# Performance work log

Measured on AMD Instinct MI355X. Metric: run time of the kernel, lower is better.

The kernel has to match this reference:

```python
import jax, jax.numpy as jnp
import numpy as np

HEAD_SIZE = 64


def setup_inputs() -> dict:
    key = jax.random.key(0)
    ks = jax.random.split(key, 10)
    B, S, D, H, hs = 4, 2048, 768, 12, HEAD_SIZE
    F = 4 * D
    sd = lambda n: 1.0 / np.sqrt(n)
    return {
        "x": jax.random.normal(ks[0], (B, S, D), jnp.float32),
        "Wq": jax.random.normal(ks[1], (H, D, hs), jnp.float32) * sd(D),
        "Wk": jax.random.normal(ks[2], (H, D, hs), jnp.float32) * sd(D),
        "Wv": jax.random.normal(ks[3], (H, D, hs), jnp.float32) * sd(D),
        "Wo": jax.random.normal(ks[4], (D, D), jnp.float32) * sd(D),
        "bo": jnp.zeros((D,), jnp.float32),
        "W1": jax.random.normal(ks[5], (D, F), jnp.float32) * sd(D),
        "b1": jnp.zeros((F,), jnp.float32),
        "W2": jax.random.normal(ks[6], (F, D), jnp.float32) * sd(F),
        "b2": jnp.zeros((D,), jnp.float32),
    }


def reference(x, Wq, Wk, Wv, Wo, bo, W1, b1, W2, b2):
    B, S, D = x.shape
    hs = Wq.shape[-1]
    # per-head projections (no bias), vectorized over heads: [B,H,S,hs]
    q = jnp.einsum("bsd,hde->bhse", x, Wq)
    k = jnp.einsum("bsd,hde->bhse", x, Wk)
    v = jnp.einsum("bsd,hde->bhse", x, Wv)
    # causal attention scores [B,H,S,S], scaled by sqrt(head_size)
    scores = jnp.einsum("bhse,bhte->bhst", q, k) / jnp.sqrt(jnp.float32(hs))
    causal = jnp.tril(jnp.ones((S, S), dtype=bool))
    scores = jnp.where(causal, scores, -jnp.inf)
    attn = jax.nn.softmax(scores, axis=-1)
    z = jnp.einsum("bhst,bhte->bhse", attn, v)
    # concat heads along feature dim (head order preserved) -> [B,S,D]
    z = z.transpose(0, 2, 1, 3).reshape(B, S, D)
    # output projection + residual
    z = z @ Wo + bo + x
    # FFN + residual
    h = jax.nn.relu(z @ W1 + b1)
    return h @ W2 + b2 + z
```

## Files before the change

kernel.cpp:

```cpp
#include <hip/hip_runtime.h>


typedef __attribute__((ext_vector_type(4))) float f32x4;
typedef __attribute__((ext_vector_type(8))) short bf16x8;
typedef __attribute__((ext_vector_type(4))) unsigned short u16x4;

#define GLB_AS __attribute__((address_space(1)))
#define LDS_AS __attribute__((address_space(3)))

__device__ __forceinline__ unsigned short f2bf(float f) {
  unsigned int u = __float_as_uint(f);
  u = (u + 0x7FFFu + ((u >> 16) & 1u)) >> 16;
  return (unsigned short)u;
}

__device__ __forceinline__ void gload16(const void* g, void* l) {
  __builtin_amdgcn_global_load_lds((const GLB_AS unsigned int*)g,
                                   (LDS_AS unsigned int*)l, 16, 0, 0);
}

__device__ __forceinline__ int xcd_swz(int orig, int nwg) {
  int q = nwg >> 3, r = nwg & 7;
  int xcd = orig & 7, rest = orig >> 3;
  return (xcd < r ? xcd * (q + 1) : r * (q + 1) + (xcd - r) * q) + rest;
}

#define VMW4 asm volatile("s_waitcnt vmcnt(4)" ::: "memory")
#define VMW0 asm volatile("s_waitcnt vmcnt(0)" ::: "memory")

__global__ void castx(const float* __restrict__ in, unsigned short* __restrict__ out, int n) {
  int i = (blockIdx.x * 256 + threadIdx.x) * 4;
  if (i < n) {
    float4 f = *(const float4*)&in[i];
    u16x4 o;
    o[0] = f2bf(f.x); o[1] = f2bf(f.y); o[2] = f2bf(f.z); o[3] = f2bf(f.w);
    *(u16x4*)&out[i] = o;
  }
}

__global__ void tcast3(const float* __restrict__ Wq, const float* __restrict__ Wk,
                       const float* __restrict__ Wv, unsigned short* __restrict__ out,
                       float qscale) {
  __shared__ float tile[32][33];
  const int R = 768, C = 64;
  int z = blockIdx.z, wsel = z / 12, head = z % 12;
  const float* in = (wsel == 0 ? Wq : wsel == 1 ? Wk : Wv) + (size_t)head * R * C;
  unsigned short* outb = out + (size_t)wsel * R * R + (size_t)head * R * C;
  float scale = wsel == 0 ? qscale : 1.0f;
  int bx = blockIdx.x * 32;
  int by = blockIdx.y * 32;
  int tx = threadIdx.x, ty = threadIdx.y;
  #pragma unroll
  for (int i = 0; i < 32; i += 8)
    tile[ty + i][tx] = in[(size_t)(by + ty + i) * C + bx + tx];
  __syncthreads();
  #pragma unroll
  for (int i = 0; i < 32; i += 8)
    outb[(size_t)(bx + ty + i) * R + by + tx] = f2bf(tile[tx][ty + i] * scale);
}

__global__ void tcastW(const float* __restrict__ Wo, const float* __restrict__ W1,
                       const float* __restrict__ W2, unsigned short* __restrict__ woT,
                       unsigned short* __restrict__ w1T, unsigned short* __restrict__ w2T) {
  __shared__ float tile[32][33];
  int id = blockIdx.x;
  const float* in; unsigned short* out; int C, gx;
  if (id < 576)       {           in = Wo; out = woT; C = 768;  gx = 24; }
  else if (id < 2880) { id -= 576;  in = W1; out = w1T; C = 3072; gx = 96; }
  else                { id -= 2880; in = W2; out = w2T; C = 768;  gx = 24; }
  int bx = (id % gx) * 32;
  int by = (id / gx) * 32;
  int tx = threadIdx.x, ty = threadIdx.y;
  #pragma unroll
  for (int i = 0; i < 32; i += 8)
    tile[ty + i][tx] = in[(size_t)(by + ty + i) * C + bx + tx];
  __syncthreads();
  int R = (C == 768 && gx == 24 && in == W2) ? 3072 : 768;
  #pragma unroll
  for (int i = 0; i < 32; i += 8)
    out[(size_t)(bx + ty + i) * R + by + tx] = f2bf(tile[tx][ty + i]);
}

template <int EPI, int MAP>
__global__ void gemm_bf16(const unsigned short* __restrict__ A,
                          const unsigned short* __restrict__ Bt,
                          const float* __restrict__ bias,
                          const float* __restrict__ resid,
                          float* __restrict__ Cf,
                          unsigned short* __restrict__ Cb,
                          unsigned short* __restrict__ Vt,
                          int M, int N, int K, int gy, size_t segN) {
  __shared__ unsigned short Alds[2][128 * 32];
  __shared__ unsigned short Blds[2][128 * 32];
  const int tid = threadIdx.x;
  const int lane = tid & 63;
  const int w = tid >> 6;
  const int wm = w & 1, wn = w >> 1;

  int bm, bn;
  if constexpr (MAP == 2) {
    const int xcd = blockIdx.x & 7, rest = blockIdx.x >> 3;
    if (rest < 128) { bm = (rest >> 1) * 128; bn = (xcd * 2 + (rest & 1)) * 128; }
    else { int r2 = rest - 128; bm = (xcd * 8 + (r2 & 7)) * 128; bn = (16 + (r2 >> 3)) * 128; }
  } else {
    const int wg = xcd_swz(blockIdx.x, gridDim.x);
    const int gsz = 8 * gy;
    const int group = wg / gsz;
    const int rem = wg - group * gsz;
    bm = (group * 8 + (rem & 7)) * 128;
    bn = (rem >> 3) * 128;
  }

  f32x4 acc[4][4] = {};

  const int r0 = tid >> 2;
  const int c0 = (tid & 3) * 8;
  const int sg8 = ((tid & 3) ^ ((r0 >> 1) & 3)) * 8;
  const int rc8 = (((lane >> 4)) ^ ((lane >> 1) & 3)) * 8;

  #pragma unroll
  for (int i = 0; i < 2; ++i) {
    int row = r0 + i * 64;
    gload16(&A[(size_t)(bm + row) * K + sg8], &Alds[0][row * 32 + c0]);
    gload16(&Bt[(size_t)(bn + row) * K + sg8], &Blds[0][row * 32 + c0]);
  }
  __syncthreads();

  int buf = 0;
  for (int k0 = 0; k0 < K; k0 += 32) {
    if (k0 + 32 < K) {
      #pragma unroll
      for (int i = 0; i < 2; ++i) {
        int row = r0 + i * 64;
        gload16(&A[(size_t)(bm + row) * K + k0 + 32 + sg8], &Alds[buf ^ 1][row * 32 + c0]);
        gload16(&Bt[(size_t)(bn + row) * K + k0 + 32 + sg8], &Blds[buf ^ 1][row * 32 + c0]);
      }
      VMW4;
    } else {
      VMW0;
    }
    __builtin_amdgcn_s_barrier();

    bf16x8 af[4], bf[4];
    #pragma unroll
    for (int m = 0; m < 4; ++m)
      af[m] = *(const bf16x8*)&Alds[buf][(wm * 64 + m * 16 + (lane & 15)) * 32 + rc8];
    #pragma unroll
    for (int n = 0; n < 4; ++n)
      bf[n] = *(const bf16x8*)&Blds[buf][(wn * 64 + n * 16 + (lane & 15)) * 32 + rc8];
    #pragma unroll
    for (int m = 0; m < 4; ++m)
      #pragma unroll
      for (int n = 0; n < 4; ++n)
        acc[m][n] = __builtin_amdgcn_mfma_f32_16x16x32_bf16(af[m], bf[n], acc[m][n], 0, 0, 0);

    __builtin_amdgcn_s_barrier();
    buf ^= 1;
  }

  const int crow0 = bm + wm * 64 + ((lane >> 4)) * 4;
  const int ccol0 = bn + wn * 64 + (lane & 15);
  const int seg = bn / 768;
  const int lcol0 = (bn % 768) + wn * 64 + (lane & 15);
  #pragma unroll
  for (int m = 0; m < 4; ++m) {
    #pragma unroll
    for (int n = 0; n < 4; ++n) {
      int col = ccol0 + n * 16;
      #pragma unroll
      for (int r = 0; r < 4; ++r) {
        int row = crow0 + m * 16 + r;
        float v = acc[m][n][r];
        if constexpr (EPI & 1) v += bias[col];
        if constexpr (EPI & 4) v += resid[(size_t)row * N + col];
        if constexpr (EPI & 2) v = fmaxf(v, 0.f);
        if constexpr (EPI & 8) Cf[(size_t)row * N + col] = v;
        if constexpr (EPI & 16) Cb[(size_t)row * N + col] = f2bf(v);
        if constexpr (EPI & 32) {
          int lc = lcol0 + n * 16;
          if ((EPI & 64) && seg == 2) {
            int hh = lc >> 6, e = lc & 63;
            int bb = row >> 11, s = row & 2047;
            Vt[((size_t)(bb * 12 + hh) * 64 + e) * 2048 + s] = f2bf(v);
          } else {
            Cb[(size_t)seg * segN + (size_t)row * 768 + lc] = f2bf(v);
          }
        }
      }
    }
  }
}

__global__ void attn_fwd(const unsigned short* __restrict__ q,
                         const unsigned short* __restrict__ k,
                         const unsigned short* __restrict__ vT,
                         unsigned short* __restrict__ z) {
  __shared__ unsigned short Klds[2 * 2 * 64 * 32];
  __shared__ unsigned short Vlds[2 * 2 * 64 * 32];
  __shared__ unsigned short Plds[4 * 16 * 72];

  const int wgid = xcd_swz(blockIdx.x, gridDim.x);
  const int pi = wgid & 15;
  const int bh = wgid >> 4;
  const int b = bh / 12, h = bh % 12;
  const int tid = threadIdx.x, lane = tid & 63, w = tid >> 6;
  const int q16 = lane & 15;
  const int qt  = lane >> 4;
  const int rdc = ((qt ^ ((q16 >> 1) & 3)) * 8);

  const int srow = tid >> 2;
  const int sdc  = (tid & 3) * 8;
  const int sgc  = (((tid & 3) ^ ((srow >> 1) & 3)) * 8);
  const size_t kbase = (size_t)(b * 2048) * 768 + h * 64;
  const size_t vbase = (size_t)((b * 12 + h) * 64) * 2048;
  unsigned short* Pw = &Plds[w * 16 * 72];

  #pragma unroll 1
  for (int seg = 0; seg < 2; ++seg) {
    const int qb = seg == 0 ? pi : 31 - pi;
    const int q0 = qb * 64;
    const int nt = qb + 1;

    const int qrow = q0 + w * 16 + q16;
    const size_t qoff = (size_t)(b * 2048 + qrow) * 768 + h * 64 + qt * 8;
    bf16x8 qf0 = *(const bf16x8*)&q[qoff];
    bf16x8 qf1 = *(const bf16x8*)&q[qoff + 32];

    f32x4 accO[4] = {};
    float lrow = 0.f;

    #pragma unroll
    for (int i = 0; i < 2; ++i) {
      gload16(&k[kbase + (size_t)srow * 768 + i * 32 + sgc],
              &Klds[i * 2048 + srow * 32 + sdc]);
      gload16(&vT[vbase + (size_t)srow * 2048 + i * 32 + sgc],
              &Vlds[i * 2048 + srow * 32 + sdc]);
    }
    __syncthreads();

    int buf = 0;
    for (int t = 0; t < nt; ++t) {
      if (t + 1 < nt) {
        const int kv1 = (t + 1) * 64;
        const int bo = (buf ^ 1) * 4096;
        #pragma unroll
        for (int i = 0; i < 2; ++i) {
          gload16(&k[kbase + (size_t)(kv1 + srow) * 768 + i * 32 + sgc],
                  &Klds[bo + i * 2048 + srow * 32 + sdc]);
          gload16(&vT[vbase + (size_t)srow * 2048 + kv1 + i * 32 + sgc],
                  &Vlds[bo + i * 2048 + srow * 32 + sdc]);
        }
        VMW4;
      } else {
        VMW0;
      }
      __builtin_amdgcn_s_barrier();

      const int kv0 = t * 64;
      const int kb_ = buf * 4096;

      bf16x8 kf0[4], kf1[4];
      #pragma unroll
      for (int n = 0; n < 4; ++n) {
        kf0[n] = *(const bf16x8*)&Klds[kb_ + 0 * 2048 + (n * 16 + q16) * 32 + rdc];
        kf1[n] = *(const bf16x8*)&Klds[kb_ + 1 * 2048 + (n * 16 + q16) * 32 + rdc];
      }
      f32x4 s[4];
      __builtin_amdgcn_s_setprio(1);
      #pragma unroll
      for (int n = 0; n < 4; ++n) {
        f32x4 zz = {};
        s[n] = __builtin_amdgcn_mfma_f32_16x16x32_bf16(kf0[n], qf0, zz, 0, 0, 0);
      }
      #pragma unroll
      for (int n = 0; n < 4; ++n)
        s[n] = __builtin_amdgcn_mfma_f32_16x16x32_bf16(kf1[n], qf1, s[n], 0, 0, 0);
      __builtin_amdgcn_s_setprio(0);

      if (t == nt - 1) {
        const int rowg = q0 + w * 16 + q16;
        #pragma unroll
        for (int n = 0; n < 4; ++n)
          #pragma unroll
          for (int r = 0; r < 4; ++r)
            if (kv0 + n * 16 + qt * 4 + r > rowg) s[n][r] = -3.0e38f;
      }

      #pragma unroll
      for (int n = 0; n < 4; ++n)
        #pragma unroll
        for (int r = 0; r < 4; ++r) { s[n][r] = exp2f(s[n][r]); lrow += s[n][r]; }

      #pragma unroll
      for (int n = 0; n < 4; ++n) {
        unsigned int lo, hi;
        asm("v_cvt_pk_bf16_f32 %0, %1, %2" : "=v"(lo) : "v"(s[n][0]), "v"(s[n][1]));
        asm("v_cvt_pk_bf16_f32 %0, %1, %2" : "=v"(hi) : "v"(s[n][2]), "v"(s[n][3]));
        uint2 pk; pk.x = lo; pk.y = hi;
        *(uint2*)&Pw[q16 * 72 + n * 16 + qt * 4] = pk;
      }

      __builtin_amdgcn_s_setprio(1);
      #pragma unroll
      for (int kk = 0; kk < 2; ++kk) {
        bf16x8 pf = *(const bf16x8*)&Pw[q16 * 72 + kk * 32 + qt * 8];
        #pragma unroll
        for (int n = 0; n < 4; ++n) {
          bf16x8 vf = *(const bf16x8*)&Vlds[kb_ + kk * 2048 + (n * 16 + q16) * 32 + rdc];
          accO[n] = __builtin_amdgcn_mfma_f32_16x16x32_bf16(pf, vf, accO[n], 0, 0, 0);
        }
      }
      __builtin_amdgcn_s_setprio(0);

      __builtin_amdgcn_s_barrier();
      buf ^= 1;
    }

    lrow += __shfl_xor(lrow, 16);
    lrow += __shfl_xor(lrow, 32);
    #pragma unroll
    for (int r = 0; r < 4; ++r) {
      float lr = __int_as_float(__builtin_amdgcn_ds_bpermute((qt * 4 + r) * 4,
                                                             __float_as_int(lrow)));
      float linv = 1.0f / lr;
      int rowg = q0 + w * 16 + qt * 4 + r;
      #pragma unroll
      for (int n = 0; n < 4; ++n)
        z[(size_t)(b * 2048 + rowg) * 768 + h * 64 + n * 16 + q16]
            = f2bf(accO[n][r] * linv);
    }
  }
}

extern "C" void kernel_launch(void* const* d_in, const int* in_sizes, int n_in,
                              void* d_out, int out_size, void* d_ws, size_t ws_size,
                              hipStream_t stream) {
  const float* x  = (const float*)d_in[0];
  const float* Wq = (const float*)d_in[1];
  const float* Wk = (const float*)d_in[2];
  const float* Wv = (const float*)d_in[3];
  const float* Wo = (const float*)d_in[4];
  const float* bo = (const float*)d_in[5];
  const float* W1 = (const float*)d_in[6];
  const float* b1 = (const float*)d_in[7];
  const float* W2 = (const float*)d_in[8];
  const float* b2 = (const float*)d_in[9];
  float* out = (float*)d_out;

  const int B = 4, S = 2048, D = 768, H = 12, hs = 64, F = 3072;
  const int M = B * S;
  const size_t MD = (size_t)M * D;

  unsigned short* xb   = (unsigned short*)d_ws;
  unsigned short* qb   = xb + MD;
  unsigned short* kb   = qb + MD;
  unsigned short* vb   = kb + MD;
  unsigned short* hbuf = xb;
  unsigned short* vT   = vb + MD;
  unsigned short* zb   = vT + MD;
  float*          z2f  = (float*)(zb + MD);
  unsigned short* z2b  = (unsigned short*)(z2f + MD);
  unsigned short* wqkvT= z2b + MD;
  unsigned short* woT  = wqkvT + 3 * (size_t)D * D;
  unsigned short* w1T  = woT + (size_t)D * D;
  unsigned short* w2T  = w1T + (size_t)D * F;

  dim3 tb(32, 8);

  castx<<<dim3((int)(MD / 4 / 256)), 256, 0, stream>>>(x, xb, (int)MD);

  const float QS = 0.125f * 1.4426950408889634f;
  tcast3<<<dim3(hs / 32, D / 32, 3 * H), tb, 0, stream>>>(Wq, Wk, Wv, wqkvT, QS);
  tcastW<<<dim3(5184), tb, 0, stream>>>(Wo, W1, W2, woT, w1T, w2T);

  {
    int gy = 3 * D / 128;
    gemm_bf16<32 | 64, 2><<<dim3(64 * gy), 256, 0, stream>>>(
        xb, wqkvT, nullptr, nullptr, nullptr, qb, vT, M, 3 * D, D, gy, MD);
  }

  attn_fwd<<<dim3((S / 128) * B * H), 256, 0, stream>>>(qb, kb, vT, zb);

  {
    int gy = D / 128;
    gemm_bf16<1 | 4 | 8 | 16, 0><<<dim3(64 * gy), 256, 0, stream>>>(
        zb, woT, bo, x, z2f, z2b, nullptr, M, D, D, gy, 0);
  }
  {
    int gy = F / 128;
    gemm_bf16<1 | 2 | 16, 0><<<dim3(64 * gy), 256, 0, stream>>>(
        z2b, w1T, b1, nullptr, nullptr, hbuf, nullptr, M, F, D, gy, 0);
  }
  {
    int gy = D / 128;
    gemm_bf16<1 | 4 | 8, 0><<<dim3(64 * gy), 256, 0, stream>>>(
        hbuf, w2T, b2, z2f, out, nullptr, nullptr, M, D, F, gy, 0);
  }
}
```

Baseline: 292.3 us.

## Triple-buffer GEMM LDS tiles and drop XOR swizzle on loads

The bf16 GEMM moves from a double-buffered to a triple-buffered LDS pipeline, prefetching three k-tiles ahead with graded vmcnt waits, to hide more global-load latency. It also removes the XOR swizzle on the global-to-LDS copy and the fragment reads, using plain linear offsets. That removal is likely to bring back LDS bank conflicts on the 16-byte fragment reads. Larger LDS use per block may also lower occupancy.

```diff
diff --git a/kernel.cpp b/kernel.cpp
--- a/kernel.cpp
+++ b/kernel.cpp
@@ -25,6 +25,7 @@
   return (xcd < r ? xcd * (q + 1) : r * (q + 1) + (xcd - r) * q) + rest;
 }
 
+#define VMW8 asm volatile("s_waitcnt vmcnt(8)" ::: "memory")
 #define VMW4 asm volatile("s_waitcnt vmcnt(4)" ::: "memory")
 #define VMW0 asm volatile("s_waitcnt vmcnt(0)" ::: "memory")
 
@@ -64,10 +65,10 @@
                        unsigned short* __restrict__ w1T, unsigned short* __restrict__ w2T) {
   __shared__ float tile[32][33];
   int id = blockIdx.x;
-  const float* in; unsigned short* out; int C, gx;
-  if (id < 576)       {           in = Wo; out = woT; C = 768;  gx = 24; }
-  else if (id < 2880) { id -= 576;  in = W1; out = w1T; C = 3072; gx = 96; }
-  else                { id -= 2880; in = W2; out = w2T; C = 768;  gx = 24; }
+  const float* in; unsigned short* out; int C, gx, R;
+  if (id < 576)       {           in = Wo; out = woT; C = 768;  gx = 24; R = 768; }
+  else if (id < 2880) { id -= 576;  in = W1; out = w1T; C = 3072; gx = 96; R = 768; }
+  else                { id -= 2880; in = W2; out = w2T; C = 768;  gx = 24; R = 3072; }
   int bx = (id % gx) * 32;
   int by = (id / gx) * 32;
   int tx = threadIdx.x, ty = threadIdx.y;
@@ -75,7 +76,6 @@
   for (int i = 0; i < 32; i += 8)
     tile[ty + i][tx] = in[(size_t)(by + ty + i) * C + bx + tx];
   __syncthreads();
-  int R = (C == 768 && gx == 24 && in == W2) ? 3072 : 768;
   #pragma unroll
   for (int i = 0; i < 32; i += 8)
     out[(size_t)(bx + ty + i) * R + by + tx] = f2bf(tile[tx][ty + i]);
@@ -90,8 +90,8 @@
                           unsigned short* __restrict__ Cb,
                           unsigned short* __restrict__ Vt,
                           int M, int N, int K, int gy, size_t segN) {
-  __shared__ unsigned short Alds[2][128 * 32];
-  __shared__ unsigned short Blds[2][128 * 32];
+  __shared__ unsigned short Alds[3][128 * 32];
+  __shared__ unsigned short Blds[3][128 * 32];
   const int tid = threadIdx.x;
   const int lane = tid & 63;
   const int w = tid >> 6;
@@ -115,47 +115,53 @@
 
   const int r0 = tid >> 2;
   const int c0 = (tid & 3) * 8;
-  const int sg8 = ((tid & 3) ^ ((r0 >> 1) & 3)) * 8;
-  const int rc8 = (((lane >> 4)) ^ ((lane >> 1) & 3)) * 8;
-
-  #pragma unroll
-  for (int i = 0; i < 2; ++i) {
-    int row = r0 + i * 64;
-    gload16(&A[(size_t)(bm + row) * K + sg8], &Alds[0][row * 32 + c0]);
-    gload16(&Bt[(size_t)(bn + row) * K + sg8], &Blds[0][row * 32 + c0]);
-  }
-  __syncthreads();
-
-  int buf = 0;
-  for (int k0 = 0; k0 < K; k0 += 32) {
-    if (k0 + 32 < K) {
+
+  #pragma unroll
+  for (int p = 0; p < 3; ++p) {
+    #pragma unroll
+    for (int i = 0; i < 2; ++i) {
+      int row = r0 + i * 64;
+      gload16(&A[(size_t)(bm + row) * K + p * 32 + c0], &Alds[p][row * 32 + c0]);
+      gload16(&Bt[(size_t)(bn + row) * K + p * 32 + c0], &Blds[p][row * 32 + c0]);
+    }
+  }
+
+  const int nt = K >> 5;
+  int bufr = 0;
+  for (int t = 0; t < nt; ++t) {
+    if (t + 2 < nt)      { VMW8; }
+    else if (t + 1 < nt) { VMW4; }
+    else                 { VMW0; }
+    __builtin_amdgcn_s_barrier();
+
+    const unsigned short* Ab = Alds[bufr];
+    const unsigned short* Bb = Blds[bufr];
+    bf16x8 af[4], bf[4];
+    #pragma unroll
+    for (int m = 0; m < 4; ++m)
+      af[m] = *(const bf16x8*)&Ab[(wm * 64 + m * 16 + (lane & 15)) * 32 + (lane >> 4) * 8];
+    #pragma unroll
+    for (int n = 0; n < 4; ++n)
+      bf[n] = *(const bf16x8*)&Bb[(wn * 64 + n * 16 + (lane & 15)) * 32 + (lane >> 4) * 8];
+    #pragma unroll
+    for (int m = 0; m < 4; ++m)
+      #pragma unroll
+      for (int n = 0; n < 4; ++n)
+        acc[m][n] = __builtin_amdgcn_mfma_f32_16x16x32_bf16(af[m], bf[n], acc[m][n], 0, 0, 0);
+
+    __builtin_amdgcn_s_barrier();
+    if (t + 3 < nt) {
+      const int kt = (t + 3) * 32;
+      unsigned short* Aw = Alds[bufr];
+      unsigned short* Bw = Blds[bufr];
       #pragma unroll
       for (int i = 0; i < 2; ++i) {
         int row = r0 + i * 64;
-        gload16(&A[(size_t)(bm + row) * K + k0 + 32 + sg8], &Alds[buf ^ 1][row * 32 + c0]);
-        gload16(&Bt[(size_t)(bn + row) * K + k0 + 32 + sg8], &Blds[buf ^ 1][row * 32 + c0]);
-      }
-      VMW4;
-    } else {
-      VMW0;
-    }
-    __builtin_amdgcn_s_barrier();
-
-    bf16x8 af[4], bf[4];
-    #pragma unroll
-    for (int m = 0; m < 4; ++m)
-      af[m] = *(const bf16x8*)&Alds[buf][(wm * 64 + m * 16 + (lane & 15)) * 32 + rc8];
-    #pragma unroll
-    for (int n = 0; n < 4; ++n)
-      bf[n] = *(const bf16x8*)&Blds[buf][(wn * 64 + n * 16 + (lane & 15)) * 32 + rc8];
-    #pragma unroll
-    for (int m = 0; m < 4; ++m)
-      #pragma unroll
-      for (int n = 0; n < 4; ++n)
-        acc[m][n] = __builtin_amdgcn_mfma_f32_16x16x32_bf16(af[m], bf[n], acc[m][n], 0, 0, 0);
-
-    __builtin_amdgcn_s_barrier();
-    buf ^= 1;
+        gload16(&A[(size_t)(bm + row) * K + kt + c0], &Aw[row * 32 + c0]);
+        gload16(&Bt[(size_t)(bn + row) * K + kt + c0], &Bw[row * 32 + c0]);
+      }
+    }
+    bufr = bufr == 2 ? 0 : bufr + 1;
   }
 
   const int crow0 = bm + wm * 64 + ((lane >> 4)) * 4;
@@ -250,7 +256,7 @@
           gload16(&vT[vbase + (size_t)srow * 2048 + kv1 + i * 32 + sgc],
                   &Vlds[bo + i * 2048 + srow * 32 + sdc]);
         }
-        VMW4;
+        asm volatile("s_waitcnt vmcnt(4)" ::: "memory");
       } else {
         VMW0;
       }
```

After: 283.0 us. 3.2% less time.

## Add 128x64-tile GEMM for N=768 projections, LDS-staged FFN1 epilogue, drop swizzle

Applied to the files above, without the earlier changes.

Adds a gemm_n64 kernel with 128x64 output tiles, used for the Wo and W2 GEMMs (N=768) so the grid doubles from 384 to 768 workgroups and fills more compute units. The FFN1 GEMM now stages its bias+ReLU bf16 output in LDS and writes rows back with 16-byte vector stores instead of scattered 2-byte stores. The XOR swizzle on LDS loads and reads is removed from the main GEMM, which may bring back LDS bank conflicts. Smaller tiles lower per-block data reuse in exchange for better occupancy.

```diff
diff --git a/kernel.cpp b/kernel.cpp
--- a/kernel.cpp
+++ b/kernel.cpp
@@ -26,6 +26,7 @@
 }
 
 #define VMW4 asm volatile("s_waitcnt vmcnt(4)" ::: "memory")
+#define VMW3 asm volatile("s_waitcnt vmcnt(3)" ::: "memory")
 #define VMW0 asm volatile("s_waitcnt vmcnt(0)" ::: "memory")
 
 __global__ void castx(const float* __restrict__ in, unsigned short* __restrict__ out, int n) {
@@ -64,10 +65,10 @@
                        unsigned short* __restrict__ w1T, unsigned short* __restrict__ w2T) {
   __shared__ float tile[32][33];
   int id = blockIdx.x;
-  const float* in; unsigned short* out; int C, gx;
-  if (id < 576)       {           in = Wo; out = woT; C = 768;  gx = 24; }
-  else if (id < 2880) { id -= 576;  in = W1; out = w1T; C = 3072; gx = 96; }
-  else                { id -= 2880; in = W2; out = w2T; C = 768;  gx = 24; }
+  const float* in; unsigned short* out; int C, gx, R;
+  if (id < 576)       {           in = Wo; out = woT; C = 768;  gx = 24; R = 768; }
+  else if (id < 2880) { id -= 576;  in = W1; out = w1T; C = 3072; gx = 96; R = 768; }
+  else                { id -= 2880; in = W2; out = w2T; C = 768;  gx = 24; R = 3072; }
   int bx = (id % gx) * 32;
   int by = (id / gx) * 32;
   int tx = threadIdx.x, ty = threadIdx.y;
@@ -75,7 +76,6 @@
   for (int i = 0; i < 32; i += 8)
     tile[ty + i][tx] = in[(size_t)(by + ty + i) * C + bx + tx];
   __syncthreads();
-  int R = (C == 768 && gx == 24 && in == W2) ? 3072 : 768;
   #pragma unroll
   for (int i = 0; i < 32; i += 8)
     out[(size_t)(bx + ty + i) * R + by + tx] = f2bf(tile[tx][ty + i]);
@@ -115,14 +115,12 @@
 
   const int r0 = tid >> 2;
   const int c0 = (tid & 3) * 8;
-  const int sg8 = ((tid & 3) ^ ((r0 >> 1) & 3)) * 8;
-  const int rc8 = (((lane >> 4)) ^ ((lane >> 1) & 3)) * 8;
 
   #pragma unroll
   for (int i = 0; i < 2; ++i) {
     int row = r0 + i * 64;
-    gload16(&A[(size_t)(bm + row) * K + sg8], &Alds[0][row * 32 + c0]);
-    gload16(&Bt[(size_t)(bn + row) * K + sg8], &Blds[0][row * 32 + c0]);
+    gload16(&A[(size_t)(bm + row) * K + c0], &Alds[0][row * 32 + c0]);
+    gload16(&Bt[(size_t)(bn + row) * K + c0], &Blds[0][row * 32 + c0]);
   }
   __syncthreads();
 
@@ -132,8 +130,8 @@
       #pragma unroll
       for (int i = 0; i < 2; ++i) {
         int row = r0 + i * 64;
-        gload16(&A[(size_t)(bm + row) * K + k0 + 32 + sg8], &Alds[buf ^ 1][row * 32 + c0]);
-        gload16(&Bt[(size_t)(bn + row) * K + k0 + 32 + sg8], &Blds[buf ^ 1][row * 32 + c0]);
+        gload16(&A[(size_t)(bm + row) * K + k0 + 32 + c0], &Alds[buf ^ 1][row * 32 + c0]);
+        gload16(&Bt[(size_t)(bn + row) * K + k0 + 32 + c0], &Blds[buf ^ 1][row * 32 + c0]);
       }
       VMW4;
     } else {
@@ -144,10 +142,10 @@
     bf16x8 af[4], bf[4];
     #pragma unroll
     for (int m = 0; m < 4; ++m)
-      af[m] = *(const bf16x8*)&Alds[buf][(wm * 64 + m * 16 + (lane & 15)) * 32 + rc8];
+      af[m] = *(const bf16x8*)&Alds[buf][(wm * 64 + m * 16 + (lane & 15)) * 32 + (lane >> 4) * 8];
     #pragma unroll
     for (int n = 0; n < 4; ++n)
-      bf[n] = *(const bf16x8*)&Blds[buf][(wn * 64 + n * 16 + (lane & 15)) * 32 + rc8];
+      bf[n] = *(const bf16x8*)&Blds[buf][(wn * 64 + n * 16 + (lane & 15)) * 32 + (lane >> 4) * 8];
     #pragma unroll
     for (int m = 0; m < 4; ++m)
       #pragma unroll
@@ -160,12 +158,136 @@
 
   const int crow0 = bm + wm * 64 + ((lane >> 4)) * 4;
   const int ccol0 = bn + wn * 64 + (lane & 15);
-  const int seg = bn / 768;
-  const int lcol0 = (bn % 768) + wn * 64 + (lane & 15);
+
+  if constexpr (EPI == (1 | 2 | 16)) {
+    unsigned short* C0 = &Alds[0][0];
+    unsigned short* C1 = &Blds[0][0];
+    #pragma unroll
+    for (int m = 0; m < 4; ++m) {
+      #pragma unroll
+      for (int n = 0; n < 4; ++n) {
+        int col = wn * 64 + n * 16 + (lane & 15);
+        #pragma unroll
+        for (int r = 0; r < 4; ++r) {
+          int rl = m * 16 + (lane >> 4) * 4 + r;
+          float v = acc[m][n][r] + bias[bn + col];
+          v = fmaxf(v, 0.f);
+          (wm ? C1 : C0)[rl * 128 + col] = f2bf(v);
+        }
+      }
+    }
+    __syncthreads();
+    const int rr = tid >> 4;
+    const int ch = (tid & 15) * 8;
+    #pragma unroll
+    for (int p = 0; p < 8; ++p) {
+      int row = p * 16 + rr;
+      bf16x8 vv = *(const bf16x8*)&(row < 64 ? C0 : C1)[(row & 63) * 128 + ch];
+      *(bf16x8*)&Cb[(size_t)(bm + row) * N + bn + ch] = vv;
+    }
+  } else {
+    const int seg = bn / 768;
+    const int lcol0 = (bn % 768) + wn * 64 + (lane & 15);
+    #pragma unroll
+    for (int m = 0; m < 4; ++m) {
+      #pragma unroll
+      for (int n = 0; n < 4; ++n) {
+        int col = ccol0 + n * 16;
+        #pragma unroll
+        for (int r = 0; r < 4; ++r) {
+          int row = crow0 + m * 16 + r;
+          float v = acc[m][n][r];
+          if constexpr (EPI & 1) v += bias[col];
+          if constexpr (EPI & 4) v += resid[(size_t)row * N + col];
+          if constexpr (EPI & 2) v = fmaxf(v, 0.f);
+          if constexpr (EPI & 8) Cf[(size_t)row * N + col] = v;
+          if constexpr (EPI & 16) Cb[(size_t)row * N + col] = f2bf(v);
+          if constexpr (EPI & 32) {
+            int lc = lcol0 + n * 16;
+            if ((EPI & 64) && seg == 2) {
+              int hh = lc >> 6, e = lc & 63;
+              int bb = row >> 11, s = row & 2047;
+              Vt[((size_t)(bb * 12 + hh) * 64 + e) * 2048 + s] = f2bf(v);
+            } else {
+              Cb[(size_t)seg * segN + (size_t)row * 768 + lc] = f2bf(v);
+            }
+          }
+        }
+      }
+    }
+  }
+}
+
+template <int EPI>
+__global__ void gemm_n64(const unsigned short* __restrict__ A,
+                         const unsigned short* __restrict__ Bt,
+                         const float* __restrict__ bias,
+                         const float* __restrict__ resid,
+                         float* __restrict__ Cf,
+                         unsigned short* __restrict__ Cb,
+                         int M, int N, int K, int gy) {
+  __shared__ unsigned short Alds[2][128 * 32];
+  __shared__ unsigned short Blds[2][64 * 32];
+  const int tid = threadIdx.x;
+  const int lane = tid & 63;
+  const int w = tid >> 6;
+  const int wm = w >> 1, wn = w & 1;
+
+  const int wg = xcd_swz(blockIdx.x, gridDim.x);
+  const int gsz = 8 * gy;
+  const int group = wg / gsz;
+  const int rem = wg - group * gsz;
+  const int bm = (group * 8 + (rem & 7)) * 128;
+  const int bn = (rem >> 3) * 64;
+
+  f32x4 acc[4][2] = {};
+
+  const int r0 = tid >> 2;
+  const int c0 = (tid & 3) * 8;
+
+  #pragma unroll
+  for (int i = 0; i < 2; ++i)
+    gload16(&A[(size_t)(bm + r0 + i * 64) * K + c0], &Alds[0][(r0 + i * 64) * 32 + c0]);
+  gload16(&Bt[(size_t)(bn + r0) * K + c0], &Blds[0][r0 * 32 + c0]);
+  __syncthreads();
+
+  int buf = 0;
+  for (int k0 = 0; k0 < K; k0 += 32) {
+    if (k0 + 32 < K) {
+      #pragma unroll
+      for (int i = 0; i < 2; ++i)
+        gload16(&A[(size_t)(bm + r0 + i * 64) * K + k0 + 32 + c0],
+                &Alds[buf ^ 1][(r0 + i * 64) * 32 + c0]);
+      gload16(&Bt[(size_t)(bn + r0) * K + k0 + 32 + c0], &Blds[buf ^ 1][r0 * 32 + c0]);
+      VMW3;
+    } else {
+      VMW0;
+    }
+    __builtin_amdgcn_s_barrier();
+
+    bf16x8 af[4], bf[2];
+    #pragma unroll
+    for (int m = 0; m < 4; ++m)
+      af[m] = *(const bf16x8*)&Alds[buf][(wm * 64 + m * 16 + (lane & 15)) * 32 + (lane >> 4) * 8];
+    #pragma unroll
+    for (int n = 0; n < 2; ++n)
+      bf[n] = *(const bf16x8*)&Blds[buf][(wn * 32 + n * 16 + (lane & 15)) * 32 + (lane >> 4) * 8];
+    #pragma unroll
+    for (int m = 0; m < 4; ++m)
+      #pragma unroll
+      for (int n = 0; n < 2; ++n)
+        acc[m][n] = __builtin_amdgcn_mfma_f32_16x16x32_bf16(af[m], bf[n], acc[m][n], 0, 0, 0);
+
+    __builtin_amdgcn_s_barrier();
+    buf ^= 1;
+  }
+
+  const int crow0 = bm + wm * 64 + (lane >> 4) * 4;
+  const int ccol0 = bn + wn * 32 + (lane & 15);
   #pragma unroll
   for (int m = 0; m < 4; ++m) {
     #pragma unroll
-    for (int n = 0; n < 4; ++n) {
+    for (int n = 0; n < 2; ++n) {
       int col = ccol0 + n * 16;
       #pragma unroll
       for (int r = 0; r < 4; ++r) {
@@ -176,16 +298,6 @@
         if constexpr (EPI & 2) v = fmaxf(v, 0.f);
         if constexpr (EPI & 8) Cf[(size_t)row * N + col] = v;
         if constexpr (EPI & 16) Cb[(size_t)row * N + col] = f2bf(v);
-        if constexpr (EPI & 32) {
-          int lc = lcol0 + n * 16;
-          if ((EPI & 64) && seg == 2) {
-            int hh = lc >> 6, e = lc & 63;
-            int bb = row >> 11, s = row & 2047;
-            Vt[((size_t)(bb * 12 + hh) * 64 + e) * 2048 + s] = f2bf(v);
-          } else {
-            Cb[(size_t)seg * segN + (size_t)row * 768 + lc] = f2bf(v);
-          }
-        }
       }
     }
   }
@@ -382,9 +494,9 @@
   attn_fwd<<<dim3((S / 128) * B * H), 256, 0, stream>>>(qb, kb, vT, zb);
 
   {
-    int gy = D / 128;
-    gemm_bf16<1 | 4 | 8 | 16, 0><<<dim3(64 * gy), 256, 0, stream>>>(
-        zb, woT, bo, x, z2f, z2b, nullptr, M, D, D, gy, 0);
+    int gy = D / 64;
+    gemm_n64<1 | 4 | 8 | 16><<<dim3(64 * gy), 256, 0, stream>>>(
+        zb, woT, bo, x, z2f, z2b, M, D, D, gy);
   }
   {
     int gy = F / 128;
@@ -392,8 +504,8 @@
         z2b, w1T, b1, nullptr, nullptr, hbuf, nullptr, M, F, D, gy, 0);
   }
   {
-    int gy = D / 128;
-    gemm_bf16<1 | 4 | 8, 0><<<dim3(64 * gy), 256, 0, stream>>>(
-        hbuf, w2T, b2, z2f, out, nullptr, nullptr, M, D, F, gy, 0);
-  }
-}
+    int gy = D / 64;
+    gemm_n64<1 | 4 | 8><<<dim3(64 * gy), 256, 0, stream>>>(
+        hbuf, w2T, b2, z2f, out, nullptr, M, D, F, gy);
+  }
+}
```

Measured after the change: 287.7 us. No clear change (-1.6%).
